# Performance work log

Hardware: AMD Instinct MI355X
Metric: run time of the kernel (lower is better)

Reference implementation:

```python
import jax, jax.numpy as jnp
import numpy as np

ALPHA = 0.15       # blend weight for merged mean vs center token
SIZE_DELTA = 0.0   # additive smoothing on cluster sizes


def setup_inputs() -> dict:
    key = jax.random.key(0)
    B, T, C = 8, 4096, 1024
    x = jax.random.normal(key, (B, T, C), dtype=jnp.float32)
    return {"x": x, "layer_idx": 0, "requested_r": 2048}


def reference(x, layer_idx, requested_r):
    B, T, C = x.shape
    K = max(1, T - int(requested_r))

    # token importance scores = squared L2 norm per token
    scores = jnp.sum(x * x, axis=-1)                      # [B, T]
    # CLS protection: force token 0 to be kept
    scores = scores.at[:, 0].set(jnp.finfo(scores.dtype).max)
    _, keep_idx = jax.lax.top_k(scores, K)                # [B, K]
    keep_idx = jnp.sort(keep_idx, axis=-1)

    # cosine nearest-kept-center assignment
    feat = x / (jnp.linalg.norm(x, axis=-1, keepdims=True) + 1e-12)  # [B, T, C]
    kept_feat = jnp.take_along_axis(feat, keep_idx[..., None], axis=1)  # [B, K, C]
    sim = jnp.einsum('bth,bkh->btk', feat, kept_feat)     # [B, T, K]
    assign_idx = jnp.argmax(sim, axis=-1)                 # [B, T]
    # force each kept center to self-assign (vectorized scatter,
    # replaces the original Python double for-loop with .item() syncs)
    b_idx = jnp.arange(B)[:, None]
    assign_idx = assign_idx.at[b_idx, keep_idx].set(jnp.arange(K)[None, :])

    # scatter-based size-weighted merge: segment mean over assigned tokens
    seg = (assign_idx + jnp.arange(B)[:, None] * K).reshape(-1)       # [B*T]
    sums = jax.ops.segment_sum(x.reshape(B * T, C), seg, num_segments=B * K)
    cnt = jax.ops.segment_sum(jnp.ones((B * T,), x.dtype), seg, num_segments=B * K)
    merged = (sums / (cnt[:, None] + SIZE_DELTA)).reshape(B, K, C)    # [B, K, C]

    x_kept = jnp.take_along_axis(x, keep_idx[..., None], axis=1)      # [B, K, C]
    out = (1.0 - ALPHA) * x_kept + ALPHA * merged
    return out
```

## Files before the change

kernel.cpp:

```cpp
#include <hip/hip_runtime.h>
#include <hip/hip_bf16.h>
#include <float.h>
#include <math.h>

constexpr int B_ = 8;
constexpr int T_ = 4096;
constexpr int C_ = 1024;
constexpr int K_ = 2048;
constexpr int MROWS = T_ - K_;

constexpr int BM = 128, BN = 128, BK = 32;
constexpr int NB = K_ / BN;
constexpr int NG = K_ / 64;
constexpr float REFINE_DELTA = 4e-4f;

typedef _Float16 f16x8 __attribute__((ext_vector_type(8)));
typedef float    f32x4 __attribute__((ext_vector_type(4)));

__device__ __forceinline__ void gload16(const ushort* g, ushort* l) {
  __builtin_amdgcn_global_load_lds(
      (const __attribute__((address_space(1))) unsigned int*)g,
      (__attribute__((address_space(3))) unsigned int*)l, 16, 0, 0);
}

__global__ __launch_bounds__(256) void split_score_kernel(
    const float* __restrict__ x, ushort* __restrict__ xh,
    double* __restrict__ sd, float* __restrict__ rnorm)
{
  int lane = threadIdx.x & 63, wave = threadIdx.x >> 6;
  int row = blockIdx.x * 4 + wave;
  size_t base = (size_t)row * C_;
  double s = 0.0;
  #pragma unroll
  for (int j = 0; j < 4; j++) {
    int i4 = j * 256 + lane * 4;
    float4 v = *reinterpret_cast<const float4*>(&x[base + i4]);
    ushort4 h;
    { _Float16 a = (_Float16)v.x; h.x = *(ushort*)&a; }
    { _Float16 a = (_Float16)v.y; h.y = *(ushort*)&a; }
    { _Float16 a = (_Float16)v.z; h.z = *(ushort*)&a; }
    { _Float16 a = (_Float16)v.w; h.w = *(ushort*)&a; }
    *reinterpret_cast<ushort4*>(&xh[base + i4]) = h;
    s += (double)v.x * v.x + (double)v.y * v.y
       + (double)v.z * v.z + (double)v.w * v.w;
  }
  #pragma unroll
  for (int off = 32; off > 0; off >>= 1) s += __shfl_down(s, off);
  if (lane == 0) {
    sd[row] = s;
    rnorm[row] = (float)(1.0 / (sqrt(s) + 1e-12));
  }
}

__global__ __launch_bounds__(256) void rank_kernel(
    const double* __restrict__ sd, int* __restrict__ flag)
{
  int b = blockIdx.y;
  __shared__ double sh[T_];
  for (int i = threadIdx.x; i < T_; i += 256)
    sh[i] = (i == 0) ? DBL_MAX : sd[b * T_ + i];
  __syncthreads();
  int tt = threadIdx.x >> 4;
  int g  = threadIdx.x & 15;
  int t  = blockIdx.x * 16 + tt;
  double key = sh[t];
  int cnt = 0;
  #pragma unroll 4
  for (int jj = 0; jj < 256; jj++) {
    int j = jj * 16 + g;
    double sj = sh[j];
    cnt += (sj > key) || (sj == key && j < t);
  }
  cnt += __shfl_xor(cnt, 1);
  cnt += __shfl_xor(cnt, 2);
  cnt += __shfl_xor(cnt, 4);
  cnt += __shfl_xor(cnt, 8);
  if (g == 0) flag[b * T_ + t] = (cnt < K_) ? 1 : 0;
}

__global__ __launch_bounds__(256) void select_kernel(
    const int* __restrict__ flag, int* __restrict__ keep_idx,
    int* __restrict__ drop_idx, int* __restrict__ assign,
    int* __restrict__ cnt, int* __restrict__ nref)
{
  int b = blockIdx.x, tid = threadIdx.x;
  __shared__ int sums[256];
  int f[16], s = 0;
  int base = b * T_ + tid * 16;
  #pragma unroll
  for (int i = 0; i < 16; i++) { f[i] = flag[base + i]; s += f[i]; }
  sums[tid] = s;
  __syncthreads();
  for (int off = 1; off < 256; off <<= 1) {
    int v = 0;
    if (tid >= off) v = sums[tid - off];
    __syncthreads();
    if (tid >= off) sums[tid] += v;
    __syncthreads();
  }
  int run = (tid == 0) ? 0 : sums[tid - 1];
  #pragma unroll
  for (int i = 0; i < 16; i++) {
    int t = tid * 16 + i;
    if (f[i]) { keep_idx[b * K_ + run] = t; assign[b * T_ + t] = run; run++; }
    else drop_idx[b * MROWS + (t - run)] = t;
  }
  #pragma unroll
  for (int i = 0; i < 8; i++) cnt[b * K_ + tid * 8 + i] = 1;
  if (b == 0 && tid == 0) *nref = 0;
}

__global__ __launch_bounds__(256) void mfma_argmax_kernel(
    const ushort* __restrict__ xh, const float* __restrict__ rnorm,
    const int* __restrict__ keep_idx, const int* __restrict__ drop_idx,
    float* __restrict__ pb, float* __restrict__ ps, int* __restrict__ pk)
{
  __shared__ __align__(16) ushort lds[2][2][4][128][8];

  int b  = blockIdx.z;
  int m0 = blockIdx.y * BM;
  int n0 = blockIdx.x * BN;
  int tid = threadIdx.x;
  int lane = tid & 63, wave = tid >> 6;
  int quad = lane >> 4, col = lane & 15;
  int wm = wave >> 1, wn = wave & 1;

  int srow = tid & 127;
  int sc8  = (tid >> 7) * 8;

  int dtok_s = drop_idx[b * MROWS + m0 + srow];
  const ushort* ga = xh + (size_t)(b * T_ + dtok_s) * C_;
  int ktok_s = keep_idx[b * K_ + n0 + srow];
  const ushort* gb = xh + (size_t)(b * T_ + ktok_s) * C_;

  int ldst = tid * 8;

  float scale[4]; int ncand[4];
  #pragma unroll
  for (int j = 0; j < 4; j++) {
    int nn = n0 + wn * 64 + j * 16 + col;
    ncand[j] = nn;
    scale[j] = rnorm[b * T_ + keep_idx[b * K_ + nn]];
  }

  f32x4 acc[4][4];
  #pragma unroll
  for (int i = 0; i < 4; i++)
    #pragma unroll
    for (int j = 0; j < 4; j++) acc[i][j] = (f32x4)0.f;

  auto issue = [&](int k0, int st) {
    ushort* base = &lds[st][0][0][0][0];
    gload16(ga + k0 + sc8,      base + ldst);
    gload16(ga + k0 + 16 + sc8, base + ldst + 2048);
    gload16(gb + k0 + sc8,      base + 4096 + ldst);
    gload16(gb + k0 + 16 + sc8, base + 4096 + ldst + 2048);
  };

  issue(0, 0);
  __syncthreads();

  for (int ks = 0; ks < C_ / BK; ks++) {
    int cur = ks & 1;
    if (ks < C_ / BK - 1) issue((ks + 1) * BK, cur ^ 1);

    f16x8 fa[4], fb[4];
    #pragma unroll
    for (int i = 0; i < 4; i++) {
      int row = wm * 64 + i * 16 + col;
      fa[i] = *reinterpret_cast<const f16x8*>(&lds[cur][0][quad][row][0]);
    }
    #pragma unroll
    for (int j = 0; j < 4; j++) {
      int row = wn * 64 + j * 16 + col;
      fb[j] = *reinterpret_cast<const f16x8*>(&lds[cur][1][quad][row][0]);
    }
    #pragma unroll
    for (int i = 0; i < 4; i++)
      #pragma unroll
      for (int j = 0; j < 4; j++)
        acc[i][j] = __builtin_amdgcn_mfma_f32_16x16x32_f16(fa[i], fb[j], acc[i][j], 0, 0, 0);
    __syncthreads();
  }

  int g = blockIdx.x * 2 + wn;
  #pragma unroll
  for (int i = 0; i < 4; i++) {
    #pragma unroll
    for (int r = 0; r < 4; r++) {
      float b1 = -FLT_MAX, b2 = -FLT_MAX; int k1 = 0;
      #pragma unroll
      for (int j = 0; j < 4; j++) {
        float v = acc[i][j][r] * scale[j];
        if (v > b1) { b2 = b1; b1 = v; k1 = ncand[j]; }
        else if (v > b2) b2 = v;
      }
      #pragma unroll
      for (int off = 1; off < 16; off <<= 1) {
        float ob1 = __shfl_xor(b1, off);
        float ob2 = __shfl_xor(b2, off);
        int   ok1 = __shfl_xor(k1, off);
        if (ob1 > b1 || (ob1 == b1 && ok1 < k1)) { b2 = fmaxf(b1, ob2); b1 = ob1; k1 = ok1; }
        else b2 = fmaxf(b2, ob1);
      }
      if (col == 0) {
        int tl = wm * 64 + i * 16 + quad * 4 + r;
        size_t p = ((size_t)(b * NG + g)) * MROWS + m0 + tl;
        pb[p] = b1; ps[p] = b2; pk[p] = k1;
      }
    }
  }
}

__global__ __launch_bounds__(256) void reduce2_kernel(
    const float* __restrict__ pb, const float* __restrict__ ps, const int* __restrict__ pk,
    const float* __restrict__ rnorm, const int* __restrict__ drop_idx,
    int* __restrict__ assign, int* __restrict__ cnt,
    int* __restrict__ rlist, int* __restrict__ nref)
{
  int idx2 = blockIdx.x * 256 + threadIdx.x;
  int b = idx2 >> 11;
  int rc = idx2 & (MROWS - 1);
  float b1 = -FLT_MAX, b2 = -FLT_MAX; int k1 = 0;
  for (int gg = 0; gg < NG; gg++) {
    size_t p = ((size_t)(b * NG + gg)) * MROWS + rc;
    float v = pb[p], s = ps[p]; int k = pk[p];
    if (v > b1) { b2 = fmaxf(b1, s); b1 = v; k1 = k; }
    else b2 = fmaxf(b2, v);
  }
  int t = drop_idx[idx2];
  assign[b * T_ + t] = k1;
  atomicAdd(&cnt[b * K_ + k1], 1);
  if ((b1 - b2) * rnorm[b * T_ + t] < REFINE_DELTA) {
    int qi = atomicAdd(nref, 1);
    rlist[qi] = idx2;
  }
}

__global__ __launch_bounds__(256) void refine_kernel(
    const float* __restrict__ x, const double* __restrict__ sd,
    const int* __restrict__ keep_idx, const int* __restrict__ drop_idx,
    const float* __restrict__ rnorm,
    const float* __restrict__ pb, const float* __restrict__ ps, const int* __restrict__ pk,
    const int* __restrict__ nref, const int* __restrict__ rlist,
    int* __restrict__ assign, int* __restrict__ cnt)
{
  int n = *nref;
  int lane = threadIdx.x & 63;
  int gwave = (blockIdx.x * blockDim.x + threadIdx.x) >> 6;
  int nwaves = (gridDim.x * blockDim.x) >> 6;
  for (int qi = gwave; qi < n; qi += nwaves) {
    int idx2 = rlist[qi];
    int b = idx2 >> 11, rc = idx2 & (MROWS - 1);
    int t = drop_idx[idx2];
    int bt = b * T_ + t;
    const float* xt = x + (size_t)bt * C_;
    const float4* xtv = reinterpret_cast<const float4*>(xt + lane * 16);
    float4 a0 = xtv[0], a1 = xtv[1], a2 = xtv[2], a3 = xtv[3];
    float pbg = -FLT_MAX, psg = -FLT_MAX; int pkg = 0;
    if (lane < NG) {
      size_t p = ((size_t)(b * NG + lane)) * MROWS + rc;
      pbg = pb[p]; psg = ps[p]; pkg = pk[p];
    }
    float b1 = pbg;
    #pragma unroll
    for (int off = 32; off > 0; off >>= 1) b1 = fmaxf(b1, __shfl_xor(b1, off));
    float thr = b1 - REFINE_DELTA / rnorm[bt];

    double bv = -DBL_MAX; int bk = 0x7fffffff;
    for (int g = 0; g < NG; g++) {
      float gpb = __shfl(pbg, g);
      if (gpb < thr) continue;
      float gps = __shfl(psg, g);
      int kfirst, kcount;
      if (gps >= thr) { kfirst = g * 64; kcount = 64; }
      else            { kfirst = __shfl(pkg, g); kcount = 1; }
      for (int jj = 0; jj < kcount; jj++) {
        int k = kfirst + jj;
        int kt = keep_idx[b * K_ + k];
        const float4* xrv = reinterpret_cast<const float4*>(
            x + ((size_t)b * T_ + kt) * C_ + lane * 16);
        float4 v0 = xrv[0], v1 = xrv[1], v2 = xrv[2], v3 = xrv[3];
        double s = (double)a0.x * v0.x + (double)a0.y * v0.y
                 + (double)a0.z * v0.z + (double)a0.w * v0.w
                 + (double)a1.x * v1.x + (double)a1.y * v1.y
                 + (double)a1.z * v1.z + (double)a1.w * v1.w
                 + (double)a2.x * v2.x + (double)a2.y * v2.y
                 + (double)a2.z * v2.z + (double)a2.w * v2.w
                 + (double)a3.x * v3.x + (double)a3.y * v3.y
                 + (double)a3.z * v3.z + (double)a3.w * v3.w;
        #pragma unroll
        for (int off = 32; off > 0; off >>= 1) s += __shfl_xor(s, off);
        s /= sqrt(sd[b * T_ + kt]);
        if (s > bv || (s == bv && k < bk)) { bv = s; bk = k; }
      }
    }
    if (lane == 0) {
      int old = assign[bt];
      if (bk != old) {
        atomicSub(&cnt[b * K_ + old], 1);
        atomicAdd(&cnt[b * K_ + bk], 1);
        assign[bt] = bk;
      }
    }
  }
}

__global__ __launch_bounds__(256) void scan_kernel(
    const int* __restrict__ cnt, int* __restrict__ offs, int* __restrict__ cursor)
{
  int b = blockIdx.x, tid = threadIdx.x;
  __shared__ int sums[256];
  int v[8], s = 0;
  int base = b * K_ + tid * 8;
  #pragma unroll
  for (int i = 0; i < 8; i++) { v[i] = cnt[base + i]; s += v[i]; }
  sums[tid] = s;
  __syncthreads();
  for (int off = 1; off < 256; off <<= 1) {
    int t2 = 0;
    if (tid >= off) t2 = sums[tid - off];
    __syncthreads();
    if (tid >= off) sums[tid] += t2;
    __syncthreads();
  }
  int run = (tid == 0) ? 0 : sums[tid - 1];
  #pragma unroll
  for (int i = 0; i < 8; i++) { offs[base + i] = run; cursor[base + i] = run; run += v[i]; }
}

__global__ void scatter_kernel(const int* __restrict__ assign,
                               int* __restrict__ cursor, int* __restrict__ lists)
{
  int i = blockIdx.x * 256 + threadIdx.x;
  int b = i >> 12, t = i & (T_ - 1);
  int p = atomicAdd(&cursor[b * K_ + assign[i]], 1);
  lists[b * T_ + p] = t;
}

__global__ __launch_bounds__(256) void merge_kernel(
    const float* __restrict__ x, const int* __restrict__ keep_idx,
    const int* __restrict__ cnt, const int* __restrict__ offs,
    const int* __restrict__ lists, float* __restrict__ out)
{
  __shared__ int toks[256];
  int b = blockIdx.y, k = blockIdx.x;
  int m = cnt[b * K_ + k], off = offs[b * K_ + k];
  const float* xb = x + (size_t)b * T_ * C_;
  int c4 = threadIdx.x * 4;
  float sx = 0.f, sy = 0.f, sz = 0.f, sw = 0.f;
  for (int basei = 0; basei < m; basei += 256) {
    int nchunk = min(256, m - basei);
    __syncthreads();
    if (threadIdx.x < nchunk) toks[threadIdx.x] = lists[b * T_ + off + basei + threadIdx.x];
    __syncthreads();
    for (int i = 0; i < nchunk; i++) {
      int tok = toks[i];
      float4 v = *reinterpret_cast<const float4*>(&xb[(size_t)tok * C_ + c4]);
      sx += v.x; sy += v.y; sz += v.z; sw += v.w;
    }
  }
  int kt = keep_idx[b * K_ + k];
  float4 xk = *reinterpret_cast<const float4*>(&xb[(size_t)kt * C_ + c4]);
  float fm = (float)m;
  float4 o;
  o.x = 0.85f * xk.x + 0.15f * (sx / fm);
  o.y = 0.85f * xk.y + 0.15f * (sy / fm);
  o.z = 0.85f * xk.z + 0.15f * (sz / fm);
  o.w = 0.85f * xk.w + 0.15f * (sw / fm);
  *reinterpret_cast<float4*>(&out[((size_t)b * K_ + k) * C_ + c4]) = o;
}

extern "C" void kernel_launch(void* const* d_in, const int* in_sizes, int n_in,
                              void* d_out, int out_size, void* d_ws, size_t ws_size,
                              hipStream_t stream)
{
  const float* x = (const float*)d_in[0];
  float* out = (float*)d_out;

  char* w = (char*)d_ws;
  ushort* xh    = (ushort*)w;  w += sizeof(ushort) * (size_t)B_ * T_ * C_;
  float* pb     = (float*)w;   w += sizeof(float) * (size_t)B_ * NG * MROWS;
  float* ps     = (float*)w;   w += sizeof(float) * (size_t)B_ * NG * MROWS;
  int*   pk     = (int*)w;     w += sizeof(int) * (size_t)B_ * NG * MROWS;
  double* sd    = (double*)w;  w += sizeof(double) * B_ * T_;
  float* rnorm  = (float*)w;   w += sizeof(float) * B_ * T_;
  int* flag     = (int*)w;     w += sizeof(int) * B_ * T_;
  int* keep_idx = (int*)w;     w += sizeof(int) * B_ * K_;
  int* drop_idx = (int*)w;     w += sizeof(int) * B_ * MROWS;
  int* assign   = (int*)w;     w += sizeof(int) * B_ * T_;
  int* cnt      = (int*)w;     w += sizeof(int) * B_ * K_;
  int* offs     = (int*)w;     w += sizeof(int) * B_ * K_;
  int* cursor   = (int*)w;     w += sizeof(int) * B_ * K_;
  int* lists    = (int*)w;     w += sizeof(int) * B_ * T_;
  int* rlist    = (int*)w;     w += sizeof(int) * B_ * MROWS;
  int* nref     = (int*)w;     w += 256;

  split_score_kernel<<<B_ * T_ / 4, 256, 0, stream>>>(x, xh, sd, rnorm);
  rank_kernel<<<dim3(T_ / 16, B_), 256, 0, stream>>>(sd, flag);
  select_kernel<<<B_, 256, 0, stream>>>(flag, keep_idx, drop_idx, assign, cnt, nref);
  mfma_argmax_kernel<<<dim3(NB, MROWS / BM, B_), 256, 0, stream>>>(
      xh, rnorm, keep_idx, drop_idx, pb, ps, pk);
  reduce2_kernel<<<B_ * MROWS / 256, 256, 0, stream>>>(
      pb, ps, pk, rnorm, drop_idx, assign, cnt, rlist, nref);
  refine_kernel<<<1024, 256, 0, stream>>>(
      x, sd, keep_idx, drop_idx, rnorm, pb, ps, pk, nref, rlist, assign, cnt);
  scan_kernel<<<B_, 256, 0, stream>>>(cnt, offs, cursor);
  scatter_kernel<<<B_ * T_ / 256, 256, 0, stream>>>(assign, cursor, lists);
  merge_kernel<<<dim3(K_, B_), 256, 0, stream>>>(x, keep_idx, cnt, offs, lists, out);
}
```

Before: 508.1 us.

## Switch similarity GEMM to 32x32x16 MFMA with 32-wide candidate groups

Replaces the 16x16x32 MFMA tiling with 32x32x16 f16 MFMA instructions, using 2x2 accumulators of 16 floats per wave, and reorganises the LDS fragment reads into two k-halves per step. The per-group argmax now covers 32 candidates, which doubles the number of groups (NG from 32 to 64). The partial best/second/index buffers and the refine kernel are changed to match, so every lane now reads one group. This aims at higher MFMA throughput and fewer LDS reads per FLOP. In exchange, the reduce pass has twice as many partials to scan, and the epilogue runs more shuffle rounds per output row.

Result: slower. 581.5 us (+14.4%).

```diff
diff --git a/kernel.cpp b/kernel.cpp
--- a/kernel.cpp
+++ b/kernel.cpp
@@ -11,11 +11,12 @@
 
 constexpr int BM = 128, BN = 128, BK = 32;
 constexpr int NB = K_ / BN;
-constexpr int NG = K_ / 64;
+constexpr int NG = K_ / 32;
 constexpr float REFINE_DELTA = 4e-4f;
 
 typedef _Float16 f16x8 __attribute__((ext_vector_type(8)));
 typedef float    f32x4 __attribute__((ext_vector_type(4)));
+typedef float    f32x16 __attribute__((ext_vector_type(16)));
 
 __device__ __forceinline__ void gload16(const ushort* g, ushort* l) {
   __builtin_amdgcn_global_load_lds(
@@ -122,7 +123,8 @@
   int n0 = blockIdx.x * BN;
   int tid = threadIdx.x;
   int lane = tid & 63, wave = tid >> 6;
-  int quad = lane >> 4, col = lane & 15;
+  int khalf = lane >> 5;
+  int c32 = lane & 31;
   int wm = wave >> 1, wn = wave & 1;
 
   int srow = tid & 127;
@@ -135,19 +137,19 @@
 
   int ldst = tid * 8;
 
-  float scale[4]; int ncand[4];
-  #pragma unroll
-  for (int j = 0; j < 4; j++) {
-    int nn = n0 + wn * 64 + j * 16 + col;
+  float scale[2]; int ncand[2];
+  #pragma unroll
+  for (int j = 0; j < 2; j++) {
+    int nn = n0 + wn * 64 + j * 32 + c32;
     ncand[j] = nn;
     scale[j] = rnorm[b * T_ + keep_idx[b * K_ + nn]];
   }
 
-  f32x4 acc[4][4];
-  #pragma unroll
-  for (int i = 0; i < 4; i++)
+  f32x16 acc[2][2];
+  #pragma unroll
+  for (int i = 0; i < 2; i++)
     #pragma unroll
-    for (int j = 0; j < 4; j++) acc[i][j] = (f32x4)0.f;
+    for (int j = 0; j < 2; j++) acc[i][j] = (f32x16)0.f;
 
   auto issue = [&](int k0, int st) {
     ushort* base = &lds[st][0][0][0][0];
@@ -164,49 +166,48 @@
     int cur = ks & 1;
     if (ks < C_ / BK - 1) issue((ks + 1) * BK, cur ^ 1);
 
-    f16x8 fa[4], fb[4];
     #pragma unroll
-    for (int i = 0; i < 4; i++) {
-      int row = wm * 64 + i * 16 + col;
-      fa[i] = *reinterpret_cast<const f16x8*>(&lds[cur][0][quad][row][0]);
+    for (int s = 0; s < 2; s++) {
+      int ch = s * 2 + khalf;
+      f16x8 fa[2], fb[2];
+      #pragma unroll
+      for (int i = 0; i < 2; i++)
+        fa[i] = *reinterpret_cast<const f16x8*>(&lds[cur][0][ch][wm * 64 + i * 32 + c32][0]);
+      #pragma unroll
+      for (int j = 0; j < 2; j++)
+        fb[j] = *reinterpret_cast<const f16x8*>(&lds[cur][1][ch][wn * 64 + j * 32 + c32][0]);
+      #pragma unroll
+      for (int i = 0; i < 2; i++)
+        #pragma unroll
+        for (int j = 0; j < 2; j++)
+          acc[i][j] = __builtin_amdgcn_mfma_f32_32x32x16_f16(fa[i], fb[j], acc[i][j], 0, 0, 0);
     }
+    __syncthreads();
+  }
+
+  #pragma unroll
+  for (int i = 0; i < 2; i++) {
     #pragma unroll
-    for (int j = 0; j < 4; j++) {
-      int row = wn * 64 + j * 16 + col;
-      fb[j] = *reinterpret_cast<const f16x8*>(&lds[cur][1][quad][row][0]);
-    }
-    #pragma unroll
-    for (int i = 0; i < 4; i++)
+    for (int j = 0; j < 2; j++) {
+      int g = blockIdx.x * 4 + wn * 2 + j;
       #pragma unroll
-      for (int j = 0; j < 4; j++)
-        acc[i][j] = __builtin_amdgcn_mfma_f32_16x16x32_f16(fa[i], fb[j], acc[i][j], 0, 0, 0);
-    __syncthreads();
-  }
-
-  int g = blockIdx.x * 2 + wn;
-  #pragma unroll
-  for (int i = 0; i < 4; i++) {
-    #pragma unroll
-    for (int r = 0; r < 4; r++) {
-      float b1 = -FLT_MAX, b2 = -FLT_MAX; int k1 = 0;
-      #pragma unroll
-      for (int j = 0; j < 4; j++) {
-        float v = acc[i][j][r] * scale[j];
-        if (v > b1) { b2 = b1; b1 = v; k1 = ncand[j]; }
-        else if (v > b2) b2 = v;
-      }
-      #pragma unroll
-      for (int off = 1; off < 16; off <<= 1) {
-        float ob1 = __shfl_xor(b1, off);
-        float ob2 = __shfl_xor(b2, off);
-        int   ok1 = __shfl_xor(k1, off);
-        if (ob1 > b1 || (ob1 == b1 && ok1 < k1)) { b2 = fmaxf(b1, ob2); b1 = ob1; k1 = ok1; }
-        else b2 = fmaxf(b2, ob1);
-      }
-      if (col == 0) {
-        int tl = wm * 64 + i * 16 + quad * 4 + r;
-        size_t p = ((size_t)(b * NG + g)) * MROWS + m0 + tl;
-        pb[p] = b1; ps[p] = b2; pk[p] = k1;
+      for (int r = 0; r < 16; r++) {
+        float b1 = acc[i][j][r] * scale[j];
+        float b2 = -FLT_MAX;
+        int k1 = ncand[j];
+        #pragma unroll
+        for (int off = 1; off < 32; off <<= 1) {
+          float ob1 = __shfl_xor(b1, off);
+          float ob2 = __shfl_xor(b2, off);
+          int   ok1 = __shfl_xor(k1, off);
+          if (ob1 > b1 || (ob1 == b1 && ok1 < k1)) { b2 = fmaxf(b1, ob2); b1 = ob1; k1 = ok1; }
+          else b2 = fmaxf(b2, ob1);
+        }
+        if (c32 == 0) {
+          int tl = wm * 64 + i * 32 + (r & 3) + 8 * (r >> 2) + 4 * khalf;
+          size_t p = ((size_t)(b * NG + g)) * MROWS + m0 + tl;
+          pb[p] = b1; ps[p] = b2; pk[p] = k1;
+        }
       }
     }
   }
@@ -257,11 +258,9 @@
     const float* xt = x + (size_t)bt * C_;
     const float4* xtv = reinterpret_cast<const float4*>(xt + lane * 16);
     float4 a0 = xtv[0], a1 = xtv[1], a2 = xtv[2], a3 = xtv[3];
-    float pbg = -FLT_MAX, psg = -FLT_MAX; int pkg = 0;
-    if (lane < NG) {
-      size_t p = ((size_t)(b * NG + lane)) * MROWS + rc;
-      pbg = pb[p]; psg = ps[p]; pkg = pk[p];
-    }
+    size_t pgp = ((size_t)(b * NG + lane)) * MROWS + rc;
+    float pbg = pb[pgp], psg = ps[pgp];
+    int pkg = pk[pgp];
     float b1 = pbg;
     #pragma unroll
     for (int off = 32; off > 0; off >>= 1) b1 = fmaxf(b1, __shfl_xor(b1, off));
@@ -273,7 +272,7 @@
       if (gpb < thr) continue;
       float gps = __shfl(psg, g);
       int kfirst, kcount;
-      if (gps >= thr) { kfirst = g * 64; kcount = 64; }
+      if (gps >= thr) { kfirst = g * 32; kcount = 32; }
       else            { kfirst = __shfl(pkg, g); kcount = 1; }
       for (int jj = 0; jj < kcount; jj++) {
         int k = kfirst + jj;
```
